# Optimization experiments

Hardware: AMD Instinct MI355X
Metric: run time of the kernel (lower is better)

## Reference

```python
import jax, jax.numpy as jnp
import numpy as np
import math

NUM_HEADS = 8
EPS = 1e-12  # torch F.normalize eps


def _l2norm(x):
    # torch F.normalize(x, dim=-1): x / max(||x||_2, eps)
    n = jnp.sqrt(jnp.sum(x * x, axis=-1, keepdims=True))
    return x / jnp.maximum(n, EPS)


def setup_inputs() -> dict:
    key = jax.random.key(0)
    ks = jax.random.split(key, 8)
    b, t, l, c = 8, 256, 24, 512
    s = 1.0 / math.sqrt(c)
    return {
        "q": jax.random.normal(ks[0], (b, t, l, c), jnp.float32),
        "kv": jax.random.normal(ks[1], (b, t, l, c), jnp.float32),
        "Wq": jax.random.normal(ks[2], (c, c), jnp.float32) * s,
        "bq": jnp.zeros((c,), jnp.float32),
        "Wkv": jax.random.normal(ks[3], (c, 2 * c), jnp.float32) * s,
        "bkv": jnp.zeros((2 * c,), jnp.float32),
        "Wg": jax.random.normal(ks[4], (c, c), jnp.float32) * s,
        "bg": jnp.zeros((c,), jnp.float32),
        "v_init": _l2norm(jax.random.normal(ks[5], (1, 1, l, c), jnp.float32) * s),
        "Wm": jax.random.normal(ks[6], (c, c), jnp.float32) * s,
        "bm": jnp.zeros((c,), jnp.float32),
    }


def reference(q, kv, Wq, bq, Wkv, bkv, Wg, bg, v_init, Wm, bm):
    b, t, l, c = q.shape
    H = NUM_HEADS
    d = c // H
    shortcut = q

    # q projection -> heads -> cosine normalize
    qh = (q @ Wq + bq).reshape(b, t, l, H, d).transpose(0, 1, 3, 2, 4)  # [b,t,H,l,d]
    qh = _l2norm(qh)

    # k, v_lin from kv projection
    kvp = kv @ Wkv + bkv                   # [b,t,l,2c]
    k_lin, v_lin = jnp.split(kvp, 2, axis=-1)
    kh = k_lin.reshape(b, t, l, H, d).transpose(0, 1, 3, 2, 4)
    kh = _l2norm(kh)

    # gated/tanh-modulated v: relu(sigmoid(Wg v_lin) * tanh(v_init))
    gate = jax.nn.sigmoid(v_lin @ Wg + bg)  # [b,t,l,c]
    vp = jnp.broadcast_to(v_init, (b, t, l, c))
    v = jax.nn.relu(gate * jnp.tanh(vp)).reshape(b, t, l, H, d).transpose(0, 1, 3, 2, 4)
    v = _l2norm(v)

    # attention (dropout in eval mode -> identity)
    atten = jnp.einsum('bthqd,bthkd->bthqk', qh, kh) / math.sqrt(d)
    atten = jax.nn.softmax(atten, axis=-1)
    x = jnp.einsum('bthqk,bthkd->bthqd', atten, v)   # [b,t,H,l,d]

    x = x.transpose(0, 1, 3, 2, 4).reshape(b, t, l, c)
    return (x @ Wm + bm) + shortcut
```

## Files before the change

### kernel.cpp

```cpp
#include <hip/hip_runtime.h>
#include <math.h>

typedef unsigned short u16;
typedef __attribute__((ext_vector_type(8))) short s16x8;
typedef __attribute__((ext_vector_type(4))) float f32x4;

#define NB 8
#define NT 256
#define NL 24
#define NC 512
#define NH 8
#define ND 64
#define NR (NB*NT*NL)
#define NBT (NB*NT)

__device__ __forceinline__ u16 f2bf(float f) {
    unsigned u = __float_as_uint(f);
    u = (u + 0x7fffu + ((u >> 16) & 1u)) >> 16;
    return (u16)u;
}
__device__ __forceinline__ float bf2f(u16 h) {
    return __uint_as_float(((unsigned)h) << 16);
}

__global__ void convert_kernel(const float* __restrict__ q, const float* __restrict__ kv,
                               const float* __restrict__ Wq, const float* __restrict__ Wkv,
                               const float* __restrict__ Wg, const float* __restrict__ Wm,
                               const float* __restrict__ v_init,
                               u16* __restrict__ qbf, u16* __restrict__ kvbf,
                               u16* __restrict__ Wq_t, u16* __restrict__ Wkv_t,
                               u16* __restrict__ Wg_t, u16* __restrict__ Wm_t,
                               float* __restrict__ tvi)
{
    const int stride = gridDim.x * blockDim.x;
    const int t0 = blockIdx.x * blockDim.x + threadIdx.x;

    const long long n4 = (long long)NR * NC / 4;
    for (long long i = t0; i < n4; i += stride) {
        float4 a = ((const float4*)q)[i];
        ushort4 oa;
        oa.x = f2bf(a.x); oa.y = f2bf(a.y); oa.z = f2bf(a.z); oa.w = f2bf(a.w);
        ((ushort4*)qbf)[i] = oa;
        float4 b = ((const float4*)kv)[i];
        ushort4 ob;
        ob.x = f2bf(b.x); ob.y = f2bf(b.y); ob.z = f2bf(b.z); ob.w = f2bf(b.w);
        ((ushort4*)kvbf)[i] = ob;
    }
    for (int e = t0; e < 512 * 512; e += stride) {
        int n = e >> 9, k = e & 511;
        Wq_t[e] = f2bf(Wq[k * 512 + n]);
        Wg_t[e] = f2bf(Wg[k * 512 + n]);
        Wm_t[e] = f2bf(Wm[k * 512 + n]);
    }
    for (int e = t0; e < 1024 * 512; e += stride) {
        int n = e >> 9, k = e & 511;
        Wkv_t[e] = f2bf(Wkv[k * 1024 + n]);
    }
    for (int e = t0; e < NL * NC; e += stride) {
        tvi[e] = tanhf(v_init[e]);
    }
}

template <int MODE>
__global__ __launch_bounds__(256)
void gemm_kernel(const u16* __restrict__ A, int lda,
                 const u16* __restrict__ Bt,
                 const float* __restrict__ bias,
                 void* __restrict__ out, int ldo,
                 const float* __restrict__ extra)
{
    __shared__ __align__(16) u16 Alds[128 * 32];
    __shared__ __align__(16) u16 Blds[128 * 32];

    const int tid = threadIdx.x;
    const int mb = blockIdx.x, nb = blockIdx.y;
    const int wave = tid >> 6, lane = tid & 63;
    const int wr = wave >> 1, wc = wave & 1;
    const int lrow = lane & 15;
    const int lko = (lane >> 4) * 8;

    f32x4 acc[4][4] = {};

    for (int k0 = 0; k0 < 512; k0 += 32) {
        __syncthreads();
#pragma unroll
        for (int c = 0; c < 2; ++c) {
            int ch = c * 256 + tid;
            int row = ch >> 2, k8 = (ch & 3) * 8;
            const u16* src = A + (size_t)(mb * 128 + row) * lda + k0 + k8;
            u16* dst = &Alds[(c * 256 + wave * 64) * 8];
            __builtin_amdgcn_global_load_lds(
                (const __attribute__((address_space(1))) void*)src,
                (__attribute__((address_space(3))) void*)dst, 16, 0, 0);
        }
#pragma unroll
        for (int c = 0; c < 2; ++c) {
            int ch = c * 256 + tid;
            int row = ch >> 2, k8 = (ch & 3) * 8;
            const u16* src = Bt + (size_t)(nb * 128 + row) * 512 + k0 + k8;
            u16* dst = &Blds[(c * 256 + wave * 64) * 8];
            __builtin_amdgcn_global_load_lds(
                (const __attribute__((address_space(1))) void*)src,
                (__attribute__((address_space(3))) void*)dst, 16, 0, 0);
        }
        asm volatile("s_waitcnt vmcnt(0)" ::: "memory");
        __syncthreads();

        s16x8 af[4], bfr[4];
#pragma unroll
        for (int m = 0; m < 4; ++m)
            af[m] = *(const s16x8*)&Alds[(wr * 64 + m * 16 + lrow) * 32 + lko];
#pragma unroll
        for (int n = 0; n < 4; ++n)
            bfr[n] = *(const s16x8*)&Blds[(wc * 64 + n * 16 + lrow) * 32 + lko];
#pragma unroll
        for (int m = 0; m < 4; ++m)
#pragma unroll
            for (int n = 0; n < 4; ++n)
                acc[m][n] = __builtin_amdgcn_mfma_f32_16x16x32_bf16(
                    af[m], bfr[n], acc[m][n], 0, 0, 0);
    }

    const int rbase = mb * 128 + wr * 64;
    const int cbase = nb * 128 + wc * 64;
#pragma unroll
    for (int m = 0; m < 4; ++m) {
#pragma unroll
        for (int n = 0; n < 4; ++n) {
            int row0 = rbase + m * 16 + ((lane >> 4) * 4);
            int col = cbase + n * 16 + (lane & 15);
            float bv = bias[col];
#pragma unroll
            for (int j = 0; j < 4; ++j) {
                int row = row0 + j;
                float v = acc[m][n][j] + bv;
                if constexpr (MODE == 0 || MODE == 1) {
                    ((u16*)out)[(size_t)row * ldo + col] = f2bf(v);
                } else if constexpr (MODE == 2) {
                    float g = 1.f / (1.f + __expf(-v));
                    float tv = extra[(row % NL) * NC + col];
                    ((u16*)out)[(size_t)row * ldo + col] = f2bf(fmaxf(g * tv, 0.f));
                } else {
                    float sc = extra[(size_t)row * NC + col];
                    ((float*)out)[(size_t)row * ldo + col] = v + sc;
                }
            }
        }
    }
}

__global__ __launch_bounds__(256)
void attn_kernel(const u16* __restrict__ qp, const u16* __restrict__ kvp,
                 const u16* __restrict__ vun, u16* __restrict__ xout)
{
    __shared__ float qs[24][65], ks[24][65], vs[24][65];
    __shared__ float Sm[24][25];
    __shared__ float nq[24], nk[24], nv[24];

    const int bt = blockIdx.x, h = blockIdx.y;
    const int tid = threadIdx.x;
    const size_t rowbase = (size_t)bt * NL;

    for (int idx = tid; idx < NL * ND; idx += 256) {
        int r = idx >> 6, c = idx & 63;
        qs[r][c] = bf2f(qp[(rowbase + r) * 512 + h * 64 + c]);
        ks[r][c] = bf2f(kvp[(rowbase + r) * 1024 + h * 64 + c]);
        vs[r][c] = bf2f(vun[(rowbase + r) * 512 + h * 64 + c]);
    }
    __syncthreads();

    if (tid < 72) {
        int m = tid / 24, r = tid % 24;
        float s = 0.f;
        if (m == 0)      for (int c = 0; c < 64; ++c) { float x = qs[r][c]; s += x * x; }
        else if (m == 1) for (int c = 0; c < 64; ++c) { float x = ks[r][c]; s += x * x; }
        else             for (int c = 0; c < 64; ++c) { float x = vs[r][c]; s += x * x; }
        float inv = 1.f / fmaxf(sqrtf(s), 1e-12f);
        if (m == 0) nq[r] = inv; else if (m == 1) nk[r] = inv; else nv[r] = inv;
    }
    __syncthreads();

    for (int idx = tid; idx < NL * ND; idx += 256) {
        int r = idx >> 6, c = idx & 63;
        vs[r][c] *= nv[r];
    }
    for (int e = tid; e < 24 * 24; e += 256) {
        int qi = e / 24, ki = e % 24;
        float s = 0.f;
        for (int c = 0; c < 64; ++c) s += qs[qi][c] * ks[ki][c];
        Sm[qi][ki] = s * nq[qi] * nk[ki] * 0.125f;
    }
    __syncthreads();

    if (tid < 24) {
        float mx = -1e30f;
        for (int k = 0; k < 24; ++k) mx = fmaxf(mx, Sm[tid][k]);
        float sum = 0.f;
        for (int k = 0; k < 24; ++k) {
            float e = __expf(Sm[tid][k] - mx);
            Sm[tid][k] = e; sum += e;
        }
        float inv = 1.f / sum;
        for (int k = 0; k < 24; ++k) Sm[tid][k] *= inv;
    }
    __syncthreads();

    for (int idx = tid; idx < NL * ND; idx += 256) {
        int qi = idx >> 6, c = idx & 63;
        float s = 0.f;
        for (int k = 0; k < 24; ++k) s += Sm[qi][k] * vs[k][c];
        xout[(rowbase + qi) * 512 + h * 64 + c] = f2bf(s);
    }
}

extern "C" void kernel_launch(void* const* d_in, const int* in_sizes, int n_in,
                              void* d_out, int out_size, void* d_ws, size_t ws_size,
                              hipStream_t stream)
{
    const float* q      = (const float*)d_in[0];
    const float* kv     = (const float*)d_in[1];
    const float* Wq     = (const float*)d_in[2];
    const float* bq     = (const float*)d_in[3];
    const float* Wkv    = (const float*)d_in[4];
    const float* bkv    = (const float*)d_in[5];
    const float* Wg     = (const float*)d_in[6];
    const float* bg     = (const float*)d_in[7];
    const float* v_init = (const float*)d_in[8];
    const float* Wm     = (const float*)d_in[9];
    const float* bm     = (const float*)d_in[10];

    char* ws = (char*)d_ws;
    const size_t SZ = (size_t)NR * NC;
    u16* buf0   = (u16*)(ws);
    u16* buf1   = (u16*)(ws + 2 * SZ);
    u16* qp     = (u16*)(ws + 4 * SZ);
    u16* kvp    = (u16*)(ws + 6 * SZ);
    char* wbase = ws + 10 * SZ;
    u16* Wq_t   = (u16*)(wbase);
    u16* Wkv_t  = (u16*)(wbase + 512 * 512 * 2);
    u16* Wg_t   = (u16*)(wbase + 512 * 512 * 2 + 1024 * 512 * 2);
    u16* Wm_t   = (u16*)(wbase + 2 * 512 * 512 * 2 + 1024 * 512 * 2);
    float* tvi  = (float*)(wbase + 3 * 512 * 512 * 2 + 1024 * 512 * 2);

    convert_kernel<<<1024, 256, 0, stream>>>(q, kv, Wq, Wkv, Wg, Wm, v_init,
                                             buf0, buf1, Wq_t, Wkv_t, Wg_t, Wm_t, tvi);

    gemm_kernel<1><<<dim3(NR / 128, 8), 256, 0, stream>>>(buf1, 512, Wkv_t, bkv,
                                                          kvp, 1024, nullptr);
    gemm_kernel<0><<<dim3(NR / 128, 4), 256, 0, stream>>>(buf0, 512, Wq_t, bq,
                                                          qp, 512, nullptr);
    gemm_kernel<2><<<dim3(NR / 128, 4), 256, 0, stream>>>(kvp + 512, 1024, Wg_t, bg,
                                                          buf1, 512, tvi);
    attn_kernel<<<dim3(NBT, NH), 256, 0, stream>>>(qp, kvp, buf1, buf0);

    gemm_kernel<3><<<dim3(NR / 128, 4), 256, 0, stream>>>(buf0, 512, Wm_t, bm,
                                                          d_out, 512, q);
}
```

Baseline: 656.5 us.

## Double-buffer GEMM LDS loads and rewrite attention with MFMA per-wave heads

The GEMM kernel now double-buffers its A/B LDS tiles, so the next k-slice's global-to-LDS loads are issued while MFMAs run on the current slice, with one barrier per iteration. The attention kernel is rewritten so each wave handles two heads of one (b,t) row. Q/K/V fragments go straight into registers, norms are reduced with cross-lane shuffles, QK^T and PV run on bf16 MFMA, and softmax is done in registers. The intent is to remove scalar FP32 LDS-bound attention work and the exposed load latency in the GEMM main loop. It adds padding to 32 rows, with clamped row reads and masking, and rounds P and normalized V to bf16, which costs some precision.

```diff
diff --git a/kernel.cpp b/kernel.cpp
--- a/kernel.cpp
+++ b/kernel.cpp
@@ -69,8 +69,8 @@
                  void* __restrict__ out, int ldo,
                  const float* __restrict__ extra)
 {
-    __shared__ __align__(16) u16 Alds[128 * 32];
-    __shared__ __align__(16) u16 Blds[128 * 32];
+    __shared__ __align__(16) u16 Alds[2][128 * 32];
+    __shared__ __align__(16) u16 Blds[2][128 * 32];
 
     const int tid = threadIdx.x;
     const int mb = blockIdx.x, nb = blockIdx.y;
@@ -81,45 +81,57 @@
 
     f32x4 acc[4][4] = {};
 
-    for (int k0 = 0; k0 < 512; k0 += 32) {
-        __syncthreads();
-#pragma unroll
-        for (int c = 0; c < 2; ++c) {
-            int ch = c * 256 + tid;
-            int row = ch >> 2, k8 = (ch & 3) * 8;
-            const u16* src = A + (size_t)(mb * 128 + row) * lda + k0 + k8;
-            u16* dst = &Alds[(c * 256 + wave * 64) * 8];
-            __builtin_amdgcn_global_load_lds(
-                (const __attribute__((address_space(1))) void*)src,
-                (__attribute__((address_space(3))) void*)dst, 16, 0, 0);
-        }
-#pragma unroll
-        for (int c = 0; c < 2; ++c) {
-            int ch = c * 256 + tid;
-            int row = ch >> 2, k8 = (ch & 3) * 8;
-            const u16* src = Bt + (size_t)(nb * 128 + row) * 512 + k0 + k8;
-            u16* dst = &Blds[(c * 256 + wave * 64) * 8];
-            __builtin_amdgcn_global_load_lds(
-                (const __attribute__((address_space(1))) void*)src,
-                (__attribute__((address_space(3))) void*)dst, 16, 0, 0);
-        }
-        asm volatile("s_waitcnt vmcnt(0)" ::: "memory");
-        __syncthreads();
+    const int row_a[2] = { tid >> 2, (256 + tid) >> 2 };
+    const int k8_a = (tid & 3) * 8;
+
+#define STAGE(buf, k0)                                                          \
+    do {                                                                        \
+        _Pragma("unroll")                                                       \
+        for (int c = 0; c < 2; ++c) {                                           \
+            const u16* srcA = A + (size_t)(mb * 128 + row_a[c]) * lda + (k0) + k8_a; \
+            u16* dstA = &Alds[buf][(c * 256 + wave * 64) * 8];                  \
+            __builtin_amdgcn_global_load_lds(                                   \
+                (const __attribute__((address_space(1))) void*)srcA,            \
+                (__attribute__((address_space(3))) void*)dstA, 16, 0, 0);       \
+        }                                                                       \
+        _Pragma("unroll")                                                       \
+        for (int c = 0; c < 2; ++c) {                                           \
+            const u16* srcB = Bt + (size_t)(nb * 128 + row_a[c]) * 512 + (k0) + k8_a; \
+            u16* dstB = &Blds[buf][(c * 256 + wave * 64) * 8];                  \
+            __builtin_amdgcn_global_load_lds(                                   \
+                (const __attribute__((address_space(1))) void*)srcB,            \
+                (__attribute__((address_space(3))) void*)dstB, 16, 0, 0);       \
+        }                                                                       \
+    } while (0)
+
+    STAGE(0, 0);
+    asm volatile("s_waitcnt vmcnt(0)" ::: "memory");
+    __builtin_amdgcn_s_barrier();
+
+    int cur = 0;
+#pragma unroll
+    for (int t = 0; t < 16; ++t) {
+        if (t < 15) STAGE(cur ^ 1, (t + 1) * 32);
 
         s16x8 af[4], bfr[4];
 #pragma unroll
         for (int m = 0; m < 4; ++m)
-            af[m] = *(const s16x8*)&Alds[(wr * 64 + m * 16 + lrow) * 32 + lko];
+            af[m] = *(const s16x8*)&Alds[cur][(wr * 64 + m * 16 + lrow) * 32 + lko];
 #pragma unroll
         for (int n = 0; n < 4; ++n)
-            bfr[n] = *(const s16x8*)&Blds[(wc * 64 + n * 16 + lrow) * 32 + lko];
+            bfr[n] = *(const s16x8*)&Blds[cur][(wc * 64 + n * 16 + lrow) * 32 + lko];
 #pragma unroll
         for (int m = 0; m < 4; ++m)
 #pragma unroll
             for (int n = 0; n < 4; ++n)
                 acc[m][n] = __builtin_amdgcn_mfma_f32_16x16x32_bf16(
                     af[m], bfr[n], acc[m][n], 0, 0, 0);
-    }
+
+        asm volatile("s_waitcnt vmcnt(0)" ::: "memory");
+        __builtin_amdgcn_s_barrier();
+        cur ^= 1;
+    }
+#undef STAGE
 
     const int rbase = mb * 128 + wr * 64;
     const int cbase = nb * 128 + wc * 64;
@@ -153,63 +165,130 @@
 void attn_kernel(const u16* __restrict__ qp, const u16* __restrict__ kvp,
                  const u16* __restrict__ vun, u16* __restrict__ xout)
 {
-    __shared__ float qs[24][65], ks[24][65], vs[24][65];
-    __shared__ float Sm[24][25];
-    __shared__ float nq[24], nk[24], nv[24];
-
-    const int bt = blockIdx.x, h = blockIdx.y;
+    __shared__ __align__(16) u16 Plds[4][32 * 32];
+    __shared__ __align__(16) u16 VTlds[4][64 * 32];
+
     const int tid = threadIdx.x;
-    const size_t rowbase = (size_t)bt * NL;
-
-    for (int idx = tid; idx < NL * ND; idx += 256) {
-        int r = idx >> 6, c = idx & 63;
-        qs[r][c] = bf2f(qp[(rowbase + r) * 512 + h * 64 + c]);
-        ks[r][c] = bf2f(kvp[(rowbase + r) * 1024 + h * 64 + c]);
-        vs[r][c] = bf2f(vun[(rowbase + r) * 512 + h * 64 + c]);
-    }
-    __syncthreads();
-
-    if (tid < 72) {
-        int m = tid / 24, r = tid % 24;
-        float s = 0.f;
-        if (m == 0)      for (int c = 0; c < 64; ++c) { float x = qs[r][c]; s += x * x; }
-        else if (m == 1) for (int c = 0; c < 64; ++c) { float x = ks[r][c]; s += x * x; }
-        else             for (int c = 0; c < 64; ++c) { float x = vs[r][c]; s += x * x; }
-        float inv = 1.f / fmaxf(sqrtf(s), 1e-12f);
-        if (m == 0) nq[r] = inv; else if (m == 1) nk[r] = inv; else nv[r] = inv;
-    }
-    __syncthreads();
-
-    for (int idx = tid; idx < NL * ND; idx += 256) {
-        int r = idx >> 6, c = idx & 63;
-        vs[r][c] *= nv[r];
-    }
-    for (int e = tid; e < 24 * 24; e += 256) {
-        int qi = e / 24, ki = e % 24;
-        float s = 0.f;
-        for (int c = 0; c < 64; ++c) s += qs[qi][c] * ks[ki][c];
-        Sm[qi][ki] = s * nq[qi] * nk[ki] * 0.125f;
-    }
-    __syncthreads();
-
-    if (tid < 24) {
-        float mx = -1e30f;
-        for (int k = 0; k < 24; ++k) mx = fmaxf(mx, Sm[tid][k]);
-        float sum = 0.f;
-        for (int k = 0; k < 24; ++k) {
-            float e = __expf(Sm[tid][k] - mx);
-            Sm[tid][k] = e; sum += e;
+    const int wave = tid >> 6, lane = tid & 63;
+    const int lr = lane & 15, lg = lane >> 4;
+    const size_t rowbase = (size_t)blockIdx.x * NL;
+    u16* P  = Plds[wave];
+    u16* VT = VTlds[wave];
+
+    for (int hh = 0; hh < 2; ++hh) {
+        const int h = wave * 2 + hh;
+
+        s16x8 qf[2][2], kf[2][2], vf[2][2];
+#pragma unroll
+        for (int m = 0; m < 2; ++m) {
+            int rq = m * 16 + lr; int r = rq > 23 ? 23 : rq;
+            const u16* q_ = qp  + (rowbase + r) * 512  + h * 64 + lg * 8;
+            const u16* k_ = kvp + (rowbase + r) * 1024 + h * 64 + lg * 8;
+            const u16* v_ = vun + (rowbase + r) * 512  + h * 64 + lg * 8;
+#pragma unroll
+            for (int ks = 0; ks < 2; ++ks) {
+                qf[m][ks] = *(const s16x8*)(q_ + ks * 32);
+                kf[m][ks] = *(const s16x8*)(k_ + ks * 32);
+                vf[m][ks] = *(const s16x8*)(v_ + ks * 32);
+            }
         }
-        float inv = 1.f / sum;
-        for (int k = 0; k < 24; ++k) Sm[tid][k] *= inv;
-    }
-    __syncthreads();
-
-    for (int idx = tid; idx < NL * ND; idx += 256) {
-        int qi = idx >> 6, c = idx & 63;
-        float s = 0.f;
-        for (int k = 0; k < 24; ++k) s += Sm[qi][k] * vs[k][c];
-        xout[(rowbase + qi) * 512 + h * 64 + c] = f2bf(s);
+
+        float invq[2], invk[2], invv[2];
+#pragma unroll
+        for (int m = 0; m < 2; ++m) {
+            float sq = 0.f, sk = 0.f, sv = 0.f;
+#pragma unroll
+            for (int ks = 0; ks < 2; ++ks)
+#pragma unroll
+                for (int j = 0; j < 8; ++j) {
+                    float a = bf2f((u16)qf[m][ks][j]); sq += a * a;
+                    float b = bf2f((u16)kf[m][ks][j]); sk += b * b;
+                    float c = bf2f((u16)vf[m][ks][j]); sv += c * c;
+                }
+            sq += __shfl_xor(sq, 16); sq += __shfl_xor(sq, 32);
+            sk += __shfl_xor(sk, 16); sk += __shfl_xor(sk, 32);
+            sv += __shfl_xor(sv, 16); sv += __shfl_xor(sv, 32);
+            invq[m] = 1.f / fmaxf(sqrtf(sq), 1e-12f);
+            invk[m] = 1.f / fmaxf(sqrtf(sk), 1e-12f);
+            invv[m] = 1.f / fmaxf(sqrtf(sv), 1e-12f);
+        }
+
+        f32x4 sc[2][2] = {};
+#pragma unroll
+        for (int m = 0; m < 2; ++m)
+#pragma unroll
+            for (int n = 0; n < 2; ++n)
+#pragma unroll
+                for (int ks = 0; ks < 2; ++ks)
+                    sc[m][n] = __builtin_amdgcn_mfma_f32_16x16x32_bf16(
+                        qf[m][ks], kf[n][ks], sc[m][n], 0, 0, 0);
+
+#pragma unroll
+        for (int m = 0; m < 2; ++m) {
+#pragma unroll
+            for (int j = 0; j < 4; ++j) {
+                float nq = __shfl(invq[m], lg * 4 + j);
+                float a0 = sc[m][0][j] * nq * invk[0] * 0.125f;
+                float a1 = (lr < 8) ? sc[m][1][j] * nq * invk[1] * 0.125f : -3.0e38f;
+                float mx = fmaxf(a0, a1);
+#pragma unroll
+                for (int d = 1; d < 16; d <<= 1) mx = fmaxf(mx, __shfl_xor(mx, d));
+                float e0 = __expf(a0 - mx);
+                float e1 = (lr < 8) ? __expf(a1 - mx) : 0.f;
+                float s = e0 + e1;
+#pragma unroll
+                for (int d = 1; d < 16; d <<= 1) s += __shfl_xor(s, d);
+                float inv = 1.f / s;
+                int r = m * 16 + lg * 4 + j;
+                P[r * 32 + lr]      = f2bf(e0 * inv);
+                P[r * 32 + 16 + lr] = f2bf(e1 * inv);
+            }
+        }
+
+#pragma unroll
+        for (int m = 0; m < 2; ++m)
+#pragma unroll
+            for (int ks = 0; ks < 2; ++ks)
+#pragma unroll
+                for (int j = 0; j < 8; ++j) {
+                    int c = ks * 32 + lg * 8 + j;
+                    int r = m * 16 + lr;
+                    VT[c * 32 + r] = f2bf(bf2f((u16)vf[m][ks][j]) * invv[m]);
+                }
+
+        asm volatile("s_waitcnt lgkmcnt(0)" ::: "memory");
+        __builtin_amdgcn_sched_barrier(0);
+
+        s16x8 pa[2], vb[4];
+#pragma unroll
+        for (int m = 0; m < 2; ++m)
+            pa[m] = *(const s16x8*)&P[(m * 16 + lr) * 32 + lg * 8];
+#pragma unroll
+        for (int n = 0; n < 4; ++n)
+            vb[n] = *(const s16x8*)&VT[(n * 16 + lr) * 32 + lg * 8];
+
+        f32x4 xa[2][4] = {};
+#pragma unroll
+        for (int m = 0; m < 2; ++m)
+#pragma unroll
+            for (int n = 0; n < 4; ++n)
+                xa[m][n] = __builtin_amdgcn_mfma_f32_16x16x32_bf16(
+                    pa[m], vb[n], xa[m][n], 0, 0, 0);
+
+#pragma unroll
+        for (int m = 0; m < 2; ++m)
+#pragma unroll
+            for (int n = 0; n < 4; ++n)
+#pragma unroll
+                for (int j = 0; j < 4; ++j) {
+                    int r = m * 16 + lg * 4 + j;
+                    if (r < 24)
+                        xout[(rowbase + r) * 512 + h * 64 + n * 16 + lr] =
+                            f2bf(xa[m][n][j]);
+                }
+
+        asm volatile("s_waitcnt lgkmcnt(0)" ::: "memory");
+        __builtin_amdgcn_sched_barrier(0);
     }
 }
 
@@ -251,7 +330,8 @@
                                                           qp, 512, nullptr);
     gemm_kernel<2><<<dim3(NR / 128, 4), 256, 0, stream>>>(kvp + 512, 1024, Wg_t, bg,
                                                           buf1, 512, tvi);
-    attn_kernel<<<dim3(NBT, NH), 256, 0, stream>>>(qp, kvp, buf1, buf0);
+
+    attn_kernel<<<dim3(NBT), 256, 0, stream>>>(qp, kvp, buf1, buf0);
 
     gemm_kernel<3><<<dim3(NR / 128, 4), 256, 0, stream>>>(buf0, 512, Wm_t, bm,
                                                           d_out, 512, q);
```

New measurement: 591.7 us. -9.9%, faster.
